# Kernel tuning notes

Hardware: AMD Instinct MI355X
Metric: run time of the kernel (lower is better)

The kernel has to match this reference:

```python
import jax, jax.numpy as jnp
import numpy as np

G, N, E = 64, 1000, 8192          # graphs, nodes/graph, edges/graph
F_IN, C, H, HID, NCLS = 128, 128, 4, 256, 2
EPS = 1e-5


def _gcn(x, src, dst, W, b):
    # GCNConv: symmetric normalization with self-loops, sum aggregation.
    h = x @ W                                              # [N, C]
    deg = jax.ops.segment_sum(jnp.ones(E, h.dtype), dst, num_segments=N) + 1.0
    dinv = jax.lax.rsqrt(deg)                              # deg^{-1/2}
    msg = h[src] * (dinv[src] * dinv[dst])[:, None]        # [E, C] gather
    out = jax.ops.segment_sum(msg, dst, num_segments=N)    # scatter-add
    out = out + h * (dinv * dinv)[:, None]                 # self-loop term
    return out + b


def _layernorm(y, g, b):
    mu = y.mean(-1, keepdims=True)
    var = ((y - mu) ** 2).mean(-1, keepdims=True)
    return (y - mu) * jax.lax.rsqrt(var + EPS) * g + b


def setup_inputs() -> dict:
    key = jax.random.key(0)
    ks = jax.random.split(key, 12)
    rn = lambda k, s: jax.random.normal(k, s, jnp.float32) * 0.05
    return dict(
        x=jax.random.normal(ks[0], (G, N, F_IN), jnp.float32),
        edge_index=jax.random.randint(ks[1], (G, 2, E), 0, N),
        W0=rn(ks[2], (F_IN, C)), b0=jnp.zeros((C,), jnp.float32),
        W1=rn(ks[3], (C, C)), b1=jnp.zeros((C,), jnp.float32),
        in_w=rn(ks[4], (3 * C, C)), in_b=jnp.zeros((3 * C,), jnp.float32),
        out_w=rn(ks[5], (C, C)), out_b=jnp.zeros((C,), jnp.float32),
        ln2_g=jnp.ones((C,), jnp.float32), ln2_b=jnp.zeros((C,), jnp.float32),
        mw1=rn(ks[6], (C, HID)), mb1=jnp.zeros((HID,), jnp.float32),
        mw2=rn(ks[7], (HID, C)), mb2=jnp.zeros((C,), jnp.float32),
        lw=rn(ks[8], (C, NCLS)), lb=jnp.zeros((NCLS,), jnp.float32),
    )


def reference(x, edge_index, W0, b0, W1, b1, in_w, in_b, out_w, out_b,
              ln2_g, ln2_b, mw1, mb1, mw2, mb2, lw, lb):
    src, dst = edge_index[:, 0, :], edge_index[:, 1, :]
    conv = jax.vmap(_gcn, in_axes=(0, 0, 0, None, None))
    h = jnp.tanh(conv(x, src, dst, W0, b0))   # [G, N, C]
    h = jnp.tanh(conv(h, src, dst, W1, b1))
    g = h.sum(axis=1)                          # SumAggregation -> [G, C]

    # MultiheadAttention, unbatched: sequence of G graph embeddings
    qkv = g @ in_w.T + in_b
    q, k, v = jnp.split(qkv, 3, axis=-1)
    d = C // H
    qh, kh, vh = (t.reshape(G, H, d) for t in (q, k, v))
    attn = jax.nn.softmax(jnp.einsum('qhd,khd->hqk', qh, kh) * (d ** -0.5), axis=-1)
    o = jnp.einsum('hqk,khd->qhd', attn, vh).reshape(G, C) @ out_w.T + out_b

    x_attend = o                               # dropout = identity (eval)
    # NOTE: original computes layer_norm1(x_attend) but immediately overwrites it.
    mlp = jnp.maximum(x_attend @ mw1 + mb1, 0.0) @ mw2 + mb2
    y = _layernorm(x_attend + mlp, ln2_g, ln2_b)
    node_repr = jnp.maximum(y, 0.0).sum(axis=0)  # [C]
    return node_repr @ lw + lb                   # [NCLS]
```

## Files before the change

kernel.cpp:

```cpp
#include <hip/hip_runtime.h>
#include <math.h>

#define Gn 64
#define Nn 1000
#define En 8192
#define Cc 128
#define HIDn 256
#define EPSf 1e-5f

typedef __attribute__((ext_vector_type(8))) short bh8;
typedef __attribute__((ext_vector_type(4))) float fx4;

__device__ __forceinline__ unsigned short f2bf(float f) {
    unsigned u = __float_as_uint(f);
    u += 0x7fffu + ((u >> 16) & 1u);
    return (unsigned short)(u >> 16);
}
__device__ __forceinline__ float bflo(unsigned u) { return __uint_as_float(u << 16); }
__device__ __forceinline__ float bfhi(unsigned u) { return __uint_as_float(u & 0xffff0000u); }

__global__ __launch_bounds__(256) void k_g0p(const int* __restrict__ ei, const float* __restrict__ X,
                                             const float* __restrict__ W0, const float* __restrict__ W1,
                                             int4* __restrict__ ninfo, int2* __restrict__ epair,
                                             float* __restrict__ pooled, float* __restrict__ repr,
                                             int* __restrict__ bars,
                                             unsigned short* __restrict__ Wt1g,
                                             unsigned short* __restrict__ Hout)
{
    __shared__ __align__(16) short Wt[128][136];
    __shared__ int wsum[4];
    int t = threadIdx.x;
    int b = blockIdx.x;

    if (b < 64) {
        int* curs = (int*)&Wt[0][0];
        float* dinv_s = (float*)((char*)&Wt[0][0] + 4096);
        int g = b;
        const int* srcp = ei + (size_t)g * 2 * En;
        const int* dstp = srcp + En;
        int lane = t & 63, wv = t >> 6;

        #pragma unroll
        for (int j = 0; j < 4; ++j) curs[t * 4 + j] = 0;
        __syncthreads();
        for (int e = t; e < En; e += 256) atomicAdd(&curs[dstp[e]], 1);
        __syncthreads();

        int base = t * 4;
        int d0 = curs[base], d1 = curs[base + 1], d2 = curs[base + 2], d3 = curs[base + 3];
        int s = d0 + d1 + d2 + d3;
        int v = s;
        #pragma unroll
        for (int off = 1; off <= 32; off <<= 1) {
            int u = __shfl_up(v, off);
            if (lane >= off) v += u;
        }
        if (lane == 63) wsum[wv] = v;
        __syncthreads();
        int woff = 0;
        #pragma unroll
        for (int w = 0; w < 4; ++w) if (w < wv) woff += wsum[w];
        int e0 = woff + v - s;
        int e1 = e0 + d0, e2 = e1 + d1, e3 = e2 + d2;
        float dv0 = rsqrtf((float)d0 + 1.f), dv1 = rsqrtf((float)d1 + 1.f);
        float dv2 = rsqrtf((float)d2 + 1.f), dv3 = rsqrtf((float)d3 + 1.f);
        curs[base] = e0; curs[base + 1] = e1; curs[base + 2] = e2; curs[base + 3] = e3;
        dinv_s[base] = dv0; dinv_s[base + 1] = dv1; dinv_s[base + 2] = dv2; dinv_s[base + 3] = dv3;
        if (base < Nn)     ninfo[g * Nn + base]     = make_int4(e0, d0, __float_as_int(dv0 * dv0), 0);
        if (base + 1 < Nn) ninfo[g * Nn + base + 1] = make_int4(e1, d1, __float_as_int(dv1 * dv1), 0);
        if (base + 2 < Nn) ninfo[g * Nn + base + 2] = make_int4(e2, d2, __float_as_int(dv2 * dv2), 0);
        if (base + 3 < Nn) ninfo[g * Nn + base + 3] = make_int4(e3, d3, __float_as_int(dv3 * dv3), 0);
        __syncthreads();

        for (int e = t; e < En; e += 256) {
            int dd = dstp[e], ss = srcp[e];
            int p = atomicAdd(&curs[dd], 1);
            float w = dinv_s[ss] * dinv_s[dd];
            epair[(size_t)g * En + p] = make_int2(ss, __float_as_int(w));
        }
        if (t < Cc) pooled[g * Cc + t] = 0.f;
        if (g == 0 && t < Cc) repr[t] = 0.f;
        if (g == 0 && t < 4) bars[t] = 0;
        return;
    }

    if (b == 1088) {
        for (int idx = t; idx < 16384; idx += 256) {
            int kI = idx >> 7, n = idx & 127;
            Wt[n][kI] = (short)f2bf(W1[idx]);
        }
        __syncthreads();
        for (int idx = t; idx < 2048; idx += 256) {
            int n = idx >> 4, kc = idx & 15;
            *(bh8*)(Wt1g + (size_t)idx * 8) = *(const bh8*)&Wt[n][kc * 8];
        }
        return;
    }

    int bb = b - 64;
    int xcd = bb & 7, gg = (bb >> 3) & 7, rblk = bb >> 6;
    int g = xcd + 8 * gg;
    for (int idx = t; idx < 16384; idx += 256) {
        int kI = idx >> 7, n = idx & 127;
        Wt[n][kI] = (short)f2bf(W0[idx]);
    }
    __syncthreads();

    int wave = t >> 6, l = t & 63;
    int lr = l & 15, lg = l >> 4;
    const float* Xf = X + (size_t)g * Nn * Cc;
    unsigned short* Hg = Hout + (size_t)g * Nn * Cc;

    int rbase = rblk * 64 + wave * 16;
    int r = rbase + lr;
    bool ok = r < Nn;
    bh8 af[4];
    #pragma unroll
    for (int ks = 0; ks < 4; ++ks) {
        if (ok) {
            const float* xp = Xf + (size_t)r * Cc + ks * 32 + lg * 8;
            fx4 a0 = *(const fx4*)xp;
            fx4 a1 = *(const fx4*)(xp + 4);
            bh8 av;
            av[0] = (short)f2bf(a0[0]); av[1] = (short)f2bf(a0[1]);
            av[2] = (short)f2bf(a0[2]); av[3] = (short)f2bf(a0[3]);
            av[4] = (short)f2bf(a1[0]); av[5] = (short)f2bf(a1[1]);
            av[6] = (short)f2bf(a1[2]); av[7] = (short)f2bf(a1[3]);
            af[ks] = av;
        } else af[ks] = bh8{0, 0, 0, 0, 0, 0, 0, 0};
    }
    fx4 acc[8];
    #pragma unroll
    for (int ct = 0; ct < 8; ++ct) acc[ct] = fx4{0.f, 0.f, 0.f, 0.f};
    #pragma unroll
    for (int ks = 0; ks < 4; ++ks) {
        #pragma unroll
        for (int ct = 0; ct < 8; ++ct) {
            bh8 bfr = *(const bh8*)(&Wt[ct * 16 + lr][ks * 32 + lg * 8]);
            acc[ct] = __builtin_amdgcn_mfma_f32_16x16x32_bf16(af[ks], bfr, acc[ct], 0, 0, 0);
        }
    }
    #pragma unroll
    for (int ct = 0; ct < 8; ++ct) {
        #pragma unroll
        for (int rg = 0; rg < 4; ++rg) {
            int row = rbase + lg * 4 + rg;
            if (row < Nn) Hg[(size_t)row * Cc + ct * 16 + lr] = f2bf(acc[ct][rg]);
        }
    }
}

__global__ __launch_bounds__(256) void k_gemm1(const unsigned short* __restrict__ Xh,
                                               const unsigned short* __restrict__ Wtg,
                                               unsigned short* __restrict__ Hout)
{
    __shared__ __align__(16) short Wt[128][136];
    int b = blockIdx.x;
    int xcd = b & 7, gg = (b >> 3) & 7, rblk = b >> 6;
    int g = xcd + 8 * gg;
    int t = threadIdx.x;
    for (int idx = t; idx < 2048; idx += 256) {
        int n = idx >> 4, kc = idx & 15;
        bh8 v = *(const bh8*)(Wtg + (size_t)idx * 8);
        *(bh8*)&Wt[n][kc * 8] = v;
    }
    __syncthreads();

    int wave = t >> 6, l = t & 63;
    int lr = l & 15, lg = l >> 4;
    const short* Xg = (const short*)Xh + (size_t)g * Nn * Cc;
    unsigned short* Hg = Hout + (size_t)g * Nn * Cc;

    int rbase = rblk * 64 + wave * 16;
    int r = rbase + lr;
    bool ok = r < Nn;
    bh8 af[4];
    #pragma unroll
    for (int ks = 0; ks < 4; ++ks) {
        if (ok) af[ks] = *(const bh8*)(Xg + (size_t)r * Cc + ks * 32 + lg * 8);
        else    af[ks] = bh8{0, 0, 0, 0, 0, 0, 0, 0};
    }
    fx4 acc[8];
    #pragma unroll
    for (int ct = 0; ct < 8; ++ct) acc[ct] = fx4{0.f, 0.f, 0.f, 0.f};
    #pragma unroll
    for (int ks = 0; ks < 4; ++ks) {
        #pragma unroll
        for (int ct = 0; ct < 8; ++ct) {
            bh8 bfr = *(const bh8*)(&Wt[ct * 16 + lr][ks * 32 + lg * 8]);
            acc[ct] = __builtin_amdgcn_mfma_f32_16x16x32_bf16(af[ks], bfr, acc[ct], 0, 0, 0);
        }
    }
    #pragma unroll
    for (int ct = 0; ct < 8; ++ct) {
        #pragma unroll
        for (int rg = 0; rg < 4; ++rg) {
            int row = rbase + lg * 4 + rg;
            if (row < Nn) Hg[(size_t)row * Cc + ct * 16 + lr] = f2bf(acc[ct][rg]);
        }
    }
}

template<int POOL>
__global__ __launch_bounds__(256) void k_combine(const unsigned* __restrict__ Hb, const int2* __restrict__ epair,
                                                 const int4* __restrict__ ninfo, const float* __restrict__ bias,
                                                 unsigned* __restrict__ Tout, float* __restrict__ pooled)
{
    int b = blockIdx.x;
    int xcd = b & 7, j = b >> 3;
    int g = xcd + 8 * (j & 7);
    int blk = j >> 3;
    int wave = threadIdx.x >> 6, lane = threadIdx.x & 63;
    const unsigned* Hg = Hb + (size_t)g * Nn * 64;
    const int2* epg = epair + (size_t)g * En;
    const int4* nig = ninfo + (size_t)g * Nn;
    float2 bb = *(const float2*)(bias + lane * 2);
    float px = 0.f, py = 0.f;
    for (int n = blk * 4 + wave; n < Nn; n += 128) {
        int4 ni = nig[n];
        int st = ni.x, dc = ni.y;
        float sw = __int_as_float(ni.z);
        unsigned hv = Hg[(size_t)n * 64 + lane];
        float a0x = bflo(hv) * sw + bb.x, a0y = bfhi(hv) * sw + bb.y;
        float a1x = 0.f, a1y = 0.f, a2x = 0.f, a2y = 0.f, a3x = 0.f, a3y = 0.f;
        int e = 0;
        for (; e + 4 <= dc; e += 4) {
            int2 p0 = epg[st + e];
            int2 p1 = epg[st + e + 1];
            int2 p2 = epg[st + e + 2];
            int2 p3 = epg[st + e + 3];
            unsigned r0 = Hg[(size_t)p0.x * 64 + lane];
            unsigned r1 = Hg[(size_t)p1.x * 64 + lane];
            unsigned r2 = Hg[(size_t)p2.x * 64 + lane];
            unsigned r3 = Hg[(size_t)p3.x * 64 + lane];
            float w0 = __int_as_float(p0.y), w1 = __int_as_float(p1.y);
            float w2 = __int_as_float(p2.y), w3 = __int_as_float(p3.y);
            a0x = fmaf(bflo(r0), w0, a0x); a0y = fmaf(bfhi(r0), w0, a0y);
            a1x = fmaf(bflo(r1), w1, a1x); a1y = fmaf(bfhi(r1), w1, a1y);
            a2x = fmaf(bflo(r2), w2, a2x); a2y = fmaf(bfhi(r2), w2, a2y);
            a3x = fmaf(bflo(r3), w3, a3x); a3y = fmaf(bfhi(r3), w3, a3y);
        }
        for (; e < dc; ++e) {
            int2 p0 = epg[st + e];
            unsigned r0 = Hg[(size_t)p0.x * 64 + lane];
            float w0 = __int_as_float(p0.y);
            a0x = fmaf(bflo(r0), w0, a0x); a0y = fmaf(bfhi(r0), w0, a0y);
        }
        float ax = (a0x + a1x) + (a2x + a3x);
        float ay = (a0y + a1y) + (a2y + a3y);
        float tx = tanhf(ax), ty = tanhf(ay);
        if (POOL) { px += tx; py += ty; }
        else Tout[(size_t)(g * Nn + n) * 64 + lane] = ((unsigned)f2bf(ty) << 16) | (unsigned)f2bf(tx);
    }
    if (POOL) {
        atomicAdd(&pooled[g * Cc + lane * 2], px);
        atomicAdd(&pooled[g * Cc + lane * 2 + 1], py);
    }
}

__global__ __launch_bounds__(1024) void k_qkv(const float* __restrict__ pooled, const float* __restrict__ in_w,
                                              const float* __restrict__ in_b, float* __restrict__ qkvb)
{
    int t = threadIdx.x, lane = t & 63, wv = t >> 6;
    int c = blockIdx.x * 16 + wv;
    const float* wr = in_w + c * Cc;
    float w0 = wr[lane], w1 = wr[64 + lane];
    float bias = in_b[c];
    for (int i = 0; i < Gn; ++i) {
        float p = fmaf(pooled[i * Cc + lane], w0, pooled[i * Cc + 64 + lane] * w1);
        #pragma unroll
        for (int off2 = 32; off2 > 0; off2 >>= 1) p += __shfl_xor(p, off2);
        if (lane == 0) qkvb[i * 384 + c] = p + bias;
    }
}

__global__ __launch_bounds__(1024) void k_attn(const float* __restrict__ qkvb, float* __restrict__ ob)
{
    __shared__ float q[64][33], kk[64][33], v[64][33];
    __shared__ float S[64][64];
    int h = blockIdx.x, t = threadIdx.x;

    for (int idx = t; idx < 2048; idx += 1024) {
        int i = idx >> 5, cc = idx & 31;
        q[i][cc]  = qkvb[i * 384 + h * 32 + cc];
        kk[i][cc] = qkvb[i * 384 + 128 + h * 32 + cc];
        v[i][cc]  = qkvb[i * 384 + 256 + h * 32 + cc];
    }
    __syncthreads();

    for (int idx = t; idx < 4096; idx += 1024) {
        int i = idx >> 6, jj = idx & 63;
        float acc = 0.f;
        #pragma unroll
        for (int d2 = 0; d2 < 32; ++d2) acc = fmaf(q[i][d2], kk[jj][d2], acc);
        S[i][jj] = acc * 0.17677669529663687f;
    }
    __syncthreads();

    int lane = t & 63, w = t >> 6;
    for (int r = w; r < 64; r += 16) {
        float val = S[r][lane];
        float m = val;
        #pragma unroll
        for (int off = 32; off > 0; off >>= 1) m = fmaxf(m, __shfl_xor(m, off));
        float e2 = expf(val - m);
        float ssum = e2;
        #pragma unroll
        for (int off = 32; off > 0; off >>= 1) ssum += __shfl_xor(ssum, off);
        S[r][lane] = e2 / ssum;
    }
    __syncthreads();

    for (int idx = t; idx < 2048; idx += 1024) {
        int i = idx >> 5, d2 = idx & 31;
        float acc = 0.f;
        #pragma unroll 4
        for (int k2 = 0; k2 < 64; ++k2) acc = fmaf(S[i][k2], v[k2][d2], acc);
        ob[i * Cc + h * 32 + d2] = acc;
    }
}

__global__ __launch_bounds__(512) void k_tailfinal(const float* __restrict__ ob, const float* __restrict__ out_w,
                                                   const float* __restrict__ out_b, const float* __restrict__ mw1,
                                                   const float* __restrict__ mb1, const float* __restrict__ mw2,
                                                   const float* __restrict__ mb2, const float* __restrict__ ln2g,
                                                   const float* __restrict__ ln2b, const float* __restrict__ lw,
                                                   const float* __restrict__ lb, float* __restrict__ repr,
                                                   int* __restrict__ ctr, float* __restrict__ out)
{
    __shared__ float sob[128];
    __shared__ float sxatt[128];
    __shared__ float sm1p[2][256];
    __shared__ float sm1[256];
    __shared__ float sp2[4][128];
    __shared__ float yb[128];
    __shared__ int slast;
    int g = blockIdx.x;
    int t = threadIdx.x, lane = t & 63, wv = t >> 6;

    if (t < 128) sob[t] = ob[(size_t)g * Cc + t];
    __syncthreads();

    {
        float o0 = sob[lane], o1 = sob[64 + lane];
        for (int c = wv; c < Cc; c += 8) {
            const float* wr = out_w + c * Cc;
            float p = fmaf(o0, wr[lane], o1 * wr[64 + lane]);
            #pragma unroll
            for (int off = 32; off > 0; off >>= 1) p += __shfl_xor(p, off);
            if (lane == 0) sxatt[c] = p + out_b[c];
        }
    }
    __syncthreads();

    {
        int jc = t & 255, half = t >> 8;
        int k0b = half * 64;
        float a[8];
        #pragma unroll
        for (int u = 0; u < 8; ++u) a[u] = 0.f;
        for (int k0 = k0b; k0 < k0b + 64; k0 += 8) {
            #pragma unroll
            for (int u = 0; u < 8; ++u)
                a[u] = fmaf(sxatt[k0 + u], mw1[(size_t)(k0 + u) * HIDn + jc], a[u]);
        }
        sm1p[half][jc] = ((a[0] + a[1]) + (a[2] + a[3])) + ((a[4] + a[5]) + (a[6] + a[7]));
        __syncthreads();
        if (t < 256) sm1[t] = fmaxf(sm1p[0][t] + sm1p[1][t] + mb1[t], 0.f);
    }
    __syncthreads();

    {
        int c = t & 127, q = t >> 7;
        int j0b = q * 64;
        float a[8];
        #pragma unroll
        for (int u = 0; u < 8; ++u) a[u] = 0.f;
        for (int j0 = j0b; j0 < j0b + 64; j0 += 8) {
            #pragma unroll
            for (int u = 0; u < 8; ++u)
                a[u] = fmaf(sm1[j0 + u], mw2[(size_t)(j0 + u) * Cc + c], a[u]);
        }
        sp2[q][c] = ((a[0] + a[1]) + (a[2] + a[3])) + ((a[4] + a[5]) + (a[6] + a[7]));
        __syncthreads();
        if (t < 128) yb[t] = sxatt[t] + (sp2[0][t] + sp2[1][t]) + (sp2[2][t] + sp2[3][t]) + mb2[t];
    }
    __syncthreads();

    if (t < 64) {
        float v0 = yb[lane], v1 = yb[64 + lane];
        float s = v0 + v1;
        #pragma unroll
        for (int off = 32; off > 0; off >>= 1) s += __shfl_xor(s, off);
        float mu = s * (1.f / 128.f);
        float d0 = v0 - mu, d1 = v1 - mu;
        float vv = d0 * d0 + d1 * d1;
        #pragma unroll
        for (int off = 32; off > 0; off >>= 1) vv += __shfl_xor(vv, off);
        float rstd = rsqrtf(vv * (1.f / 128.f) + EPSf);
        float z0 = fmaxf(d0 * rstd * ln2g[lane] + ln2b[lane], 0.f);
        float z1 = fmaxf(d1 * rstd * ln2g[64 + lane] + ln2b[64 + lane], 0.f);
        atomicAdd(&repr[lane], z0);
        atomicAdd(&repr[64 + lane], z1);
    }

    __threadfence();
    __syncthreads();
    if (t == 0) slast = atomicAdd(ctr, 1);
    __syncthreads();
    if (slast == 63) {
        __threadfence();
        __shared__ float r0s[128], r1s[128];
        if (t < 128) {
            float r = __hip_atomic_load(&repr[t], __ATOMIC_RELAXED, __HIP_MEMORY_SCOPE_AGENT);
            r0s[t] = r * lw[t * 2 + 0];
            r1s[t] = r * lw[t * 2 + 1];
        }
        __syncthreads();
        for (int s2 = 64; s2 > 0; s2 >>= 1) {
            if (t < s2) { r0s[t] += r0s[t + s2]; r1s[t] += r1s[t + s2]; }
            __syncthreads();
        }
        if (t == 0) { out[0] = r0s[0] + lb[0]; out[1] = r1s[0] + lb[1]; }
    }
}

extern "C" void kernel_launch(void* const* d_in, const int* in_sizes, int n_in,
                              void* d_out, int out_size, void* d_ws, size_t ws_size,
                              hipStream_t stream)
{
    const float* x     = (const float*)d_in[0];
    const int*   ei    = (const int*)d_in[1];
    const float* W0    = (const float*)d_in[2];
    const float* b0    = (const float*)d_in[3];
    const float* W1    = (const float*)d_in[4];
    const float* b1    = (const float*)d_in[5];
    const float* in_w  = (const float*)d_in[6];
    const float* in_b  = (const float*)d_in[7];
    const float* out_w = (const float*)d_in[8];
    const float* out_b = (const float*)d_in[9];
    const float* ln2g  = (const float*)d_in[10];
    const float* ln2b  = (const float*)d_in[11];
    const float* mw1   = (const float*)d_in[12];
    const float* mb1   = (const float*)d_in[13];
    const float* mw2   = (const float*)d_in[14];
    const float* mb2   = (const float*)d_in[15];
    const float* lw    = (const float*)d_in[16];
    const float* lb    = (const float*)d_in[17];
    float* out = (float*)d_out;
    (void)in_sizes; (void)n_in; (void)out_size; (void)ws_size;

    char* ws = (char*)d_ws;
    size_t off = 0;
    auto carve = [&](size_t bytes) { size_t o = off; off += (bytes + 255) & ~(size_t)255; return o; };
    size_t o_ni    = carve((size_t)Gn * Nn * 16);
    size_t o_ep    = carve((size_t)Gn * En * 8);
    size_t o_pool  = carve((size_t)Gn * Cc * 4);
    size_t o_qkv   = carve((size_t)Gn * 384 * 4);
    size_t o_ob    = carve((size_t)Gn * Cc * 4);
    size_t o_repr  = carve((size_t)Cc * 4);
    size_t o_bars  = carve(256);
    size_t o_W1t   = carve((size_t)Cc * Cc * 2);
    size_t o_H     = carve((size_t)Gn * Nn * Cc * 2);
    size_t o_T     = carve((size_t)Gn * Nn * Cc * 2);

    int4*  ninfo  = (int4*)(ws + o_ni);
    int2*  epair  = (int2*)(ws + o_ep);
    float* pooled = (float*)(ws + o_pool);
    float* qkvb   = (float*)(ws + o_qkv);
    float* ob     = (float*)(ws + o_ob);
    float* repr   = (float*)(ws + o_repr);
    int*   bars   = (int*)(ws + o_bars);
    unsigned short* Wt1g = (unsigned short*)(ws + o_W1t);
    unsigned short* H  = (unsigned short*)(ws + o_H);
    unsigned short* T  = (unsigned short*)(ws + o_T);

    k_g0p<<<1089, 256, 0, stream>>>(ei, x, W0, W1, ninfo, epair, pooled, repr, bars, Wt1g, H);
    k_combine<0><<<2048, 256, 0, stream>>>((const unsigned*)H, epair, ninfo, b0, (unsigned*)T, nullptr);
    k_gemm1<<<1024, 256, 0, stream>>>(T, Wt1g, H);
    k_combine<1><<<2048, 256, 0, stream>>>((const unsigned*)H, epair, ninfo, b1, nullptr, pooled);
    k_qkv<<<24, 1024, 0, stream>>>(pooled, in_w, in_b, qkvb);
    k_attn<<<4, 1024, 0, stream>>>(qkvb, ob);
    k_tailfinal<<<64, 512, 0, stream>>>(ob, out_w, out_b, mw1, mb1, mw2, mb2, ln2g, ln2b,
                                        lw, lb, repr, &bars[2], out);
}
```

Measured before the change: 159.7 us.

## Precompute bf16 W0 transpose once and use 512-thread front blocks

Moves the W0 fp32-to-bf16 transpose into a tiny separate kernel, alongside W1, so each GEMM block copies a prepacked bf16 tile instead of converting 16K floats itself. The front kernel now runs 512-thread blocks, with 128 rows per block for the GEMM and two nodes per thread in the CSR build, halving the block count. This cuts the redundant per-block weight conversion but adds an extra kernel launch ahead of the front kernel.

Result: no change. 160.1 us (+0.3%).

```diff
diff --git a/kernel.cpp b/kernel.cpp
--- a/kernel.cpp
+++ b/kernel.cpp
@@ -19,16 +19,34 @@
 __device__ __forceinline__ float bflo(unsigned u) { return __uint_as_float(u << 16); }
 __device__ __forceinline__ float bfhi(unsigned u) { return __uint_as_float(u & 0xffff0000u); }
 
-__global__ __launch_bounds__(256) void k_g0p(const int* __restrict__ ei, const float* __restrict__ X,
-                                             const float* __restrict__ W0, const float* __restrict__ W1,
-                                             int4* __restrict__ ninfo, int2* __restrict__ epair,
-                                             float* __restrict__ pooled, float* __restrict__ repr,
-                                             int* __restrict__ bars,
-                                             unsigned short* __restrict__ Wt1g,
-                                             unsigned short* __restrict__ Hout)
+__global__ __launch_bounds__(256) void k_wt(const float* __restrict__ W0, const float* __restrict__ W1,
+                                            unsigned short* __restrict__ Wt0g,
+                                            unsigned short* __restrict__ Wt1g)
+{
+    __shared__ __align__(16) short Wls[128][136];
+    int t = threadIdx.x;
+    const float* Wsrc = (blockIdx.x == 0) ? W0 : W1;
+    unsigned short* Wdst = (blockIdx.x == 0) ? Wt0g : Wt1g;
+    for (int idx = t; idx < 16384; idx += 256) {
+        int kI = idx >> 7, n = idx & 127;
+        Wls[n][kI] = (short)f2bf(Wsrc[idx]);
+    }
+    __syncthreads();
+    for (int idx = t; idx < 2048; idx += 256) {
+        int n = idx >> 4, kc = idx & 15;
+        *(bh8*)(Wdst + (size_t)idx * 8) = *(const bh8*)&Wls[n][kc * 8];
+    }
+}
+
+__global__ __launch_bounds__(512) void k_front(const int* __restrict__ ei, const float* __restrict__ X,
+                                               const unsigned short* __restrict__ Wt0g,
+                                               int4* __restrict__ ninfo, int2* __restrict__ epair,
+                                               float* __restrict__ pooled, float* __restrict__ repr,
+                                               int* __restrict__ bars,
+                                               unsigned short* __restrict__ Hout)
 {
     __shared__ __align__(16) short Wt[128][136];
-    __shared__ int wsum[4];
+    __shared__ int wsum[8];
     int t = threadIdx.x;
     int b = blockIdx.x;
 
@@ -40,15 +58,14 @@
         const int* dstp = srcp + En;
         int lane = t & 63, wv = t >> 6;
 
-        #pragma unroll
-        for (int j = 0; j < 4; ++j) curs[t * 4 + j] = 0;
-        __syncthreads();
-        for (int e = t; e < En; e += 256) atomicAdd(&curs[dstp[e]], 1);
-        __syncthreads();
-
-        int base = t * 4;
-        int d0 = curs[base], d1 = curs[base + 1], d2 = curs[base + 2], d3 = curs[base + 3];
-        int s = d0 + d1 + d2 + d3;
+        curs[t * 2] = 0; curs[t * 2 + 1] = 0;
+        __syncthreads();
+        for (int e = t; e < En; e += 512) atomicAdd(&curs[dstp[e]], 1);
+        __syncthreads();
+
+        int base = t * 2;
+        int d0 = curs[base], d1 = curs[base + 1];
+        int s = d0 + d1;
         int v = s;
         #pragma unroll
         for (int off = 1; off <= 32; off <<= 1) {
@@ -59,20 +76,17 @@
         __syncthreads();
         int woff = 0;
         #pragma unroll
-        for (int w = 0; w < 4; ++w) if (w < wv) woff += wsum[w];
+        for (int w = 0; w < 8; ++w) if (w < wv) woff += wsum[w];
         int e0 = woff + v - s;
-        int e1 = e0 + d0, e2 = e1 + d1, e3 = e2 + d2;
+        int e1 = e0 + d0;
         float dv0 = rsqrtf((float)d0 + 1.f), dv1 = rsqrtf((float)d1 + 1.f);
-        float dv2 = rsqrtf((float)d2 + 1.f), dv3 = rsqrtf((float)d3 + 1.f);
-        curs[base] = e0; curs[base + 1] = e1; curs[base + 2] = e2; curs[base + 3] = e3;
-        dinv_s[base] = dv0; dinv_s[base + 1] = dv1; dinv_s[base + 2] = dv2; dinv_s[base + 3] = dv3;
+        curs[base] = e0; curs[base + 1] = e1;
+        dinv_s[base] = dv0; dinv_s[base + 1] = dv1;
         if (base < Nn)     ninfo[g * Nn + base]     = make_int4(e0, d0, __float_as_int(dv0 * dv0), 0);
         if (base + 1 < Nn) ninfo[g * Nn + base + 1] = make_int4(e1, d1, __float_as_int(dv1 * dv1), 0);
-        if (base + 2 < Nn) ninfo[g * Nn + base + 2] = make_int4(e2, d2, __float_as_int(dv2 * dv2), 0);
-        if (base + 3 < Nn) ninfo[g * Nn + base + 3] = make_int4(e3, d3, __float_as_int(dv3 * dv3), 0);
-        __syncthreads();
-
-        for (int e = t; e < En; e += 256) {
+        __syncthreads();
+
+        for (int e = t; e < En; e += 512) {
             int dd = dstp[e], ss = srcp[e];
             int p = atomicAdd(&curs[dd], 1);
             float w = dinv_s[ss] * dinv_s[dd];
@@ -84,25 +98,12 @@
         return;
     }
 
-    if (b == 1088) {
-        for (int idx = t; idx < 16384; idx += 256) {
-            int kI = idx >> 7, n = idx & 127;
-            Wt[n][kI] = (short)f2bf(W1[idx]);
-        }
-        __syncthreads();
-        for (int idx = t; idx < 2048; idx += 256) {
-            int n = idx >> 4, kc = idx & 15;
-            *(bh8*)(Wt1g + (size_t)idx * 8) = *(const bh8*)&Wt[n][kc * 8];
-        }
-        return;
-    }
-
     int bb = b - 64;
     int xcd = bb & 7, gg = (bb >> 3) & 7, rblk = bb >> 6;
     int g = xcd + 8 * gg;
-    for (int idx = t; idx < 16384; idx += 256) {
-        int kI = idx >> 7, n = idx & 127;
-        Wt[n][kI] = (short)f2bf(W0[idx]);
+    for (int idx = t; idx < 2048; idx += 512) {
+        int n = idx >> 4, kc = idx & 15;
+        *(bh8*)&Wt[n][kc * 8] = *(const bh8*)(Wt0g + (size_t)idx * 8);
     }
     __syncthreads();
 
@@ -111,7 +112,7 @@
     const float* Xf = X + (size_t)g * Nn * Cc;
     unsigned short* Hg = Hout + (size_t)g * Nn * Cc;
 
-    int rbase = rblk * 64 + wave * 16;
+    int rbase = rblk * 128 + wave * 16;
     int r = rbase + lr;
     bool ok = r < Nn;
     bh8 af[4];
@@ -460,6 +461,7 @@
     size_t o_ob    = carve((size_t)Gn * Cc * 4);
     size_t o_repr  = carve((size_t)Cc * 4);
     size_t o_bars  = carve(256);
+    size_t o_W0t   = carve((size_t)Cc * Cc * 2);
     size_t o_W1t   = carve((size_t)Cc * Cc * 2);
     size_t o_H     = carve((size_t)Gn * Nn * Cc * 2);
     size_t o_T     = carve((size_t)Gn * Nn * Cc * 2);
@@ -471,11 +473,13 @@
     float* ob     = (float*)(ws + o_ob);
     float* repr   = (float*)(ws + o_repr);
     int*   bars   = (int*)(ws + o_bars);
+    unsigned short* Wt0g = (unsigned short*)(ws + o_W0t);
     unsigned short* Wt1g = (unsigned short*)(ws + o_W1t);
     unsigned short* H  = (unsigned short*)(ws + o_H);
     unsigned short* T  = (unsigned short*)(ws + o_T);
 
-    k_g0p<<<1089, 256, 0, stream>>>(ei, x, W0, W1, ninfo, epair, pooled, repr, bars, Wt1g, H);
+    k_wt<<<2, 256, 0, stream>>>(W0, W1, Wt0g, Wt1g);
+    k_front<<<576, 512, 0, stream>>>(ei, x, Wt0g, ninfo, epair, pooled, repr, bars, H);
     k_combine<0><<<2048, 256, 0, stream>>>((const unsigned*)H, epair, ninfo, b0, (unsigned*)T, nullptr);
     k_gemm1<<<1024, 256, 0, stream>>>(T, Wt1g, H);
     k_combine<1><<<2048, 256, 0, stream>>>((const unsigned*)H, epair, ninfo, b1, nullptr, pooled);
```
